# Optimization experiments

Hardware: AMD Instinct MI355X
Metric: run time of the kernel (lower is better)

Reference implementation:

```python
import jax, jax.numpy as jnp
import numpy as np

N = 50000      # nodes
E = 800000     # edges
D = 128        # hidden dim (args.dim) == num_features
B = 5          # GIN blocks
G = 512        # graphs in batch
C = 10         # classes
EPS_GIN = 128.0  # GINConv(nn, in_channels) -> eps = in_channels = 128 (faithful to source)
BN_EPS = 1e-5


def setup_inputs() -> dict:
    key = jax.random.key(0)
    ks = jax.random.split(key, 12)
    xav = 0.1  # ~xavier_uniform std for 128x128
    x = jax.random.normal(ks[0], (N, D), jnp.float32)
    edge_index = jax.random.randint(ks[1], (2, E), 0, N, dtype=jnp.int64)
    batch = jax.random.randint(ks[2], (N,), 0, G, dtype=jnp.int64)
    return dict(
        x=x, edge_index=edge_index, batch=batch,
        W1=jax.random.normal(ks[3], (B, D, D), jnp.float32) * xav,
        b1=jnp.zeros((B, D), jnp.float32),
        g1=jnp.ones((B, D), jnp.float32),
        be1=jnp.zeros((B, D), jnp.float32),
        W2=jax.random.normal(ks[4], (B, D, D), jnp.float32) * xav,
        b2=jnp.zeros((B, D), jnp.float32),
        g2=jnp.ones((B, D), jnp.float32),
        be2=jnp.zeros((B, D), jnp.float32),
        bn_g=jnp.ones((B * D,), jnp.float32),
        bn_b=jnp.zeros((B * D,), jnp.float32),
        Wc1=jax.random.normal(ks[5], (B * D, D), jnp.float32) * 0.05,
        bc1=jnp.zeros((D,), jnp.float32),
        Wc2=jax.random.normal(ks[6], (D, C), jnp.float32) * 0.1,
        bc2=jnp.zeros((C,), jnp.float32),
    )


def _bn(h, g, b):
    # training-mode BatchNorm1d: biased variance over the batch (node/graph) dim
    mu = h.mean(axis=0)
    var = h.var(axis=0)
    return g * (h - mu) * jax.lax.rsqrt(var + BN_EPS) + b


def reference(x, edge_index, batch, W1, b1, g1, be1, W2, b2, g2, be2,
              bn_g, bn_b, Wc1, bc1, Wc2, bc2):
    src, dst = edge_index[0], edge_index[1]
    feats = []
    for i in range(B):
        # GIN aggregation: out[dst] += x[src]
        agg = jax.ops.segment_sum(x[src], dst, num_segments=N)   # [N, D]
        h = (1.0 + EPS_GIN) * x + agg
        h = _bn(jax.nn.relu(h @ W1[i] + b1[i]), g1[i], be1[i])
        h = _bn(jax.nn.relu(h @ W2[i] + b2[i]), g2[i], be2[i])
        x = h
        # global_add_pool per graph
        feats.append(jax.ops.segment_sum(x, batch, num_segments=G))  # [G, D]
    f = jnp.concatenate(feats, axis=1)          # [G, B*D]
    f = _bn(f, bn_g, bn_b)
    f = jax.nn.relu(f @ Wc1 + bc1)              # dropout p=0 (eval)
    logits = f @ Wc2 + bc2                      # [G, C]
    return jax.nn.log_softmax(logits, axis=-1)
```

## Files before the change

kernel.cpp:

```cpp
#include <hip/hip_runtime.h>
#include <hip/hip_bf16.h>

#define NN 50000
#define NE 800000
#define DD 128
#define NB 5
#define NG 512
#define NC 10
#define BN_EPS 1e-5f
#define EPS1 129.0f
#define GATHER_BLOCKS 12500

typedef __hip_bfloat16 bf16;
typedef __attribute__((ext_vector_type(8))) short short8;
typedef __attribute__((ext_vector_type(4))) float f32x4;

__device__ __forceinline__ float b2f(const bf16 v) { return __bfloat162float(v); }
__device__ __forceinline__ float us2f(unsigned int s) {
    return __uint_as_float((s & 0xffffu) << 16);
}
__device__ __forceinline__ unsigned pack2(float a, float b) {
    union { bf16 h; unsigned short u; } ua, ub;
    ua.h = __float2bfloat16(a); ub.h = __float2bfloat16(b);
    return ((unsigned)ub.u << 16) | (unsigned)ua.u;
}
__device__ __forceinline__ short f2bfs(float f) {
    union { bf16 h; short s; } u; u.h = __float2bfloat16(f); return u.s;
}

#define OFF_AGGH   0
#define OFF_XF     3200000
#define OFF_H1     6400000
#define OFF_FEATS  9600000
#define OFF_CSA    9927680
#define OFF_CSB    9927936
#define OFF_SC6    9928192
#define OFF_SH6    9928832
#define OFF_FLAGS  9929472
#define OFF_PARAMS 9929480
#define OFF_DEG    10055680
#define OFF_OFFS   10105680
#define OFF_ELIST  10155712
#define OFF_BDEG   10955712
#define OFF_BOFFS  10956224
#define OFF_RANK   10956800
#define OFF_PART   11006800
#define OFF_ERANK  11006864

#define P_W1T  0
#define P_W2T  81920
#define P_WC1  163840
#define P_B1   245760
#define P_G1   246400
#define P_BE1  247040
#define P_B2   247680
#define P_G2   248320
#define P_BE2  248960
#define P_BNG  249600
#define P_BNB  250240
#define P_BC1  250880
#define P_WC2  251008
#define P_BC2  252288

struct SmallSrc { const void* s[11]; };

__global__ void k_detect(const unsigned* __restrict__ xw, const int* __restrict__ eiw,
                         const int* __restrict__ bw, int* flags, int* __restrict__ bdeg) {
    __shared__ int sh[3];
    const int t = threadIdx.x;
    bdeg[t] = 0; bdeg[256 + t] = 0;
    if (t < 3) sh[t] = 0;
    __syncthreads();
    int c = 0;
    for (int i = 0; i < 16; i++) {
        unsigned w = xw[t * 16 + i];
        unsigned e = (w >> 7) & 0xff;
        c += (e >= 110 && e <= 131) ? 1 : 0;
    }
    atomicAdd(&sh[0], c);
    atomicAdd(&sh[1], (eiw[2 * t + 1] != 0) ? 1 : 0);
    atomicAdd(&sh[2], (bw[2 * t + 1] != 0) ? 1 : 0);
    __syncthreads();
    if (t == 0) {
        flags[0] = (sh[0] > 2048) ? 1 : 0;
        flags[1] = (sh[1] < 8) ? 1 : 0;
        flags[2] = (sh[2] < 8) ? 1 : 0;
    }
}

__global__ void k_bhist(const int* __restrict__ flags, const int* __restrict__ batch,
                        int* __restrict__ bdeg, int* __restrict__ deg) {
    int n = blockIdx.x * 256 + threadIdx.x;
    if (n >= NN) return;
    deg[n] = 0;
    int g = flags[2] ? batch[2 * n] : batch[n];
    atomicAdd(&bdeg[g], 1);
}

__launch_bounds__(512)
__global__ void k_bscan(int* __restrict__ bdeg, int* __restrict__ boffs) {
    __shared__ int part[512];
    const int t = threadIdx.x;
    int d0 = bdeg[t];
    part[t] = d0;
    __syncthreads();
    for (int d = 1; d < 512; d <<= 1) {
        int v = (t >= d) ? part[t - d] : 0;
        __syncthreads();
        part[t] += v;
        __syncthreads();
    }
    int ex = part[t] - d0;
    boffs[t] = ex;
    bdeg[t] = ex;
    if (t == 511) boffs[512] = part[511];
}

__global__ void k_bplace(const int* __restrict__ flags, const int* __restrict__ batch,
                         int* __restrict__ bcur, int* __restrict__ rank) {
    int n = blockIdx.x * 256 + threadIdx.x;
    if (n >= NN) return;
    int g = flags[2] ? batch[2 * n] : batch[n];
    rank[n] = atomicAdd(&bcur[g], 1);
}

__global__ void k_convert_x(const int* __restrict__ flags, const void* __restrict__ xr,
                            const int* __restrict__ rank, bf16* __restrict__ xfh) {
    int i = blockIdx.x * 256 + threadIdx.x;
    int r = i >> 4, seg = i & 15;
    uint4 o;
    if (flags[0]) {
        o = ((const uint4*)xr)[i];
    } else {
        float4 a = ((const float4*)xr)[2 * i], b = ((const float4*)xr)[2 * i + 1];
        o.x = pack2(a.x, a.y); o.y = pack2(a.z, a.w);
        o.z = pack2(b.x, b.y); o.w = pack2(b.z, b.w);
    }
    ((uint4*)xfh)[(long)rank[r] * 16 + seg] = o;
}

__global__ void k_convert_params(const int* __restrict__ flags, const void* w1,
                                 const void* w2, const void* wc1, SmallSrc srcs,
                                 bf16* __restrict__ pb) {
    int i = blockIdx.x * 256 + threadIdx.x;
    if (i < 245760) {
        int which = i / 81920, j = i % 81920;
        const void* src = (which == 0) ? w1 : (which == 1) ? w2 : wc1;
        float v = flags[0] ? us2f(((const unsigned short*)src)[j]) : ((const float*)src)[j];
        if (which == 2) {
            pb[P_WC1 + j] = __float2bfloat16(v);
        } else {
            int layer = j >> 14, rem = j & 16383;
            int k = rem >> 7, c = rem & 127;
            bf16* dst = pb + (which == 0 ? P_W1T : P_W2T);
            dst[(layer << 14) + c * DD + k] = __float2bfloat16(v);
        }
    } else {
        int j = i - 245760;
        if (j >= 6538) return;
        int seg, off;
        if (j < 5120)      { seg = j / 640; off = j - seg * 640; }
        else if (j < 5248) { seg = 8;  off = j - 5120; }
        else if (j < 6528) { seg = 9;  off = j - 5248; }
        else               { seg = 10; off = j - 6528; }
        const void* s = srcs.s[seg];
        float v = flags[0] ? us2f(((const unsigned short*)s)[off]) : ((const float*)s)[off];
        pb[P_B1 + j] = __float2bfloat16(v);
    }
}

__global__ void k_hist(const int* __restrict__ flags, const int* __restrict__ ei,
                       const int* __restrict__ rank, int* __restrict__ deg,
                       int* __restrict__ erank) {
    int e = blockIdx.x * 256 + threadIdx.x;
    int d = flags[1] ? ei[2 * NE + 2 * e] : ei[NE + e];
    erank[e] = atomicAdd(&deg[rank[d]], 1);
}

__global__ void k_scan_part(const int* __restrict__ deg, int* __restrict__ part) {
    __shared__ int red[256];
    const int b = blockIdx.x, t = threadIdx.x;
    int i0 = b * 1024 + t * 4;
    int s = 0;
    if (i0 + 3 < NN) {
        int4 v = *(const int4*)(deg + i0);
        s = v.x + v.y + v.z + v.w;
    } else {
        for (int k = 0; k < 4; k++) if (i0 + k < NN) s += deg[i0 + k];
    }
    red[t] = s;
    __syncthreads();
    for (int d = 128; d > 0; d >>= 1) {
        if (t < d) red[t] += red[t + d];
        __syncthreads();
    }
    if (t == 0) part[b] = red[0];
}

__global__ void k_scan_apply(const int* __restrict__ deg, const int* __restrict__ part,
                             int* __restrict__ offs) {
    __shared__ int red[256];
    __shared__ int base_sh, total_sh;
    const int b = blockIdx.x, t = threadIdx.x;
    if (t < 64) {
        int v = (t < 49) ? part[t] : 0;
        int s = v;
        for (int d = 1; d < 64; d <<= 1) {
            int x = __shfl_up(s, d);
            if (t >= d) s += x;
        }
        if (t == b)  base_sh = s - v;
        if (t == 48) total_sh = s;
    }
    int i0 = b * 1024 + t * 4;
    int v[4]; int s = 0;
    #pragma unroll
    for (int k = 0; k < 4; k++) {
        int idx = i0 + k;
        v[k] = (idx < NN) ? deg[idx] : 0;
        s += v[k];
    }
    red[t] = s;
    __syncthreads();
    for (int d = 1; d < 256; d <<= 1) {
        int x = (t >= d) ? red[t - d] : 0;
        __syncthreads();
        red[t] += x;
        __syncthreads();
    }
    if (b == 0 && t == 0) offs[NN] = total_sh;
    int pre = base_sh + ((t == 0) ? 0 : red[t - 1]);
    #pragma unroll
    for (int k = 0; k < 4; k++) {
        int idx = i0 + k;
        if (idx < NN) { offs[idx] = pre; pre += v[k]; }
    }
}

__global__ void k_place(const int* __restrict__ flags, const int* __restrict__ ei,
                        const int* __restrict__ rank, const int* __restrict__ offs,
                        const int* __restrict__ erank, int* __restrict__ elist) {
    int e = blockIdx.x * 256 + threadIdx.x;
    int s, d;
    if (flags[1]) { s = ei[2 * e]; d = ei[2 * NE + 2 * e]; }
    else          { s = ei[e];     d = ei[NE + e]; }
    elist[offs[rank[d]] + erank[e]] = rank[s];
}

__device__ __forceinline__ void pool_body(int g, int t, const bf16* __restrict__ xfh,
                                          const int* __restrict__ boffs,
                                          const float* __restrict__ csB,
                                          const bf16* __restrict__ g2,
                                          const bf16* __restrict__ be2,
                                          float* __restrict__ feats_blk) {
    __shared__ float2 red[3][64];
    const int l = t & 63;
    const int h = t >> 6;
    const int lo = boffs[g], hi = boffs[g + 1];
    const unsigned* xw = (const unsigned*)xfh;
    float s0 = 0.f, s1 = 0.f;
    for (int n = lo + h; n < hi; n += 4) {
        unsigned p = xw[(long)n * 64 + l];
        s0 += us2f(p); s1 += us2f(p >> 16);
    }
    if (h) red[h - 1][l] = make_float2(s0, s1);
    __syncthreads();
    if (h == 0) {
        s0 += red[0][l].x + red[1][l].x + red[2][l].x;
        s1 += red[0][l].y + red[1][l].y + red[2][l].y;
        int c = l * 2;
        float mu0 = csB[c] * (1.f / NN);
        float var0 = csB[128 + c] * (1.f / NN) - mu0 * mu0;
        float sc0 = b2f(g2[c]) * rsqrtf(var0 + BN_EPS);
        float sh0 = b2f(be2[c]) - mu0 * sc0;
        float mu1 = csB[c + 1] * (1.f / NN);
        float var1 = csB[128 + c + 1] * (1.f / NN) - mu1 * mu1;
        float sc1 = b2f(g2[c + 1]) * rsqrtf(var1 + BN_EPS);
        float sh1 = b2f(be2[c + 1]) - mu1 * sc1;
        float cnt = (float)(hi - lo);
        float* fp = feats_blk + (long)g * (NB * DD) + c;
        fp[0] = sc0 * s0 + cnt * sh0;
        fp[1] = sc1 * s1 + cnt * sh1;
    }
}

__global__ void k_gather_pool(const int* __restrict__ offs, const int* __restrict__ elist,
                              const bf16* __restrict__ xfh, bf16* __restrict__ aggh,
                              const float* __restrict__ csB, const bf16* __restrict__ g2,
                              const bf16* __restrict__ be2, float* __restrict__ csA_zero,
                              const int* __restrict__ boffs, float* __restrict__ feats_prev) {
    if (blockIdx.x >= GATHER_BLOCKS) {
        if (feats_prev)
            pool_body(blockIdx.x - GATHER_BLOCKS, threadIdx.x, xfh, boffs,
                      csB, g2, be2, feats_prev);
        return;
    }
    if (blockIdx.x == 0) csA_zero[threadIdx.x] = 0.f;
    const int w = threadIdx.x >> 6;
    const int lane = threadIdx.x & 63;
    const int half = lane >> 5;
    const int ql = lane & 31;
    const int n = blockIdx.x * 4 + w;
    const int base = offs[n], end = offs[n + 1];
    const uint2* xw2 = (const uint2*)xfh;

    float a0, a1, a2, a3;
    {
        uint2 sp = xw2[(long)n * 32 + ql];
        float m = (half == 0) ? EPS1 : 0.f;
        a0 = m * us2f(sp.x); a1 = m * us2f(sp.x >> 16);
        a2 = m * us2f(sp.y); a3 = m * us2f(sp.y >> 16);
    }

    for (int i = base; i < end; i += 64) {
        int cnt = min(64, end - i);
        int e = (i + lane < end) ? elist[i + lane] : 0;
        int j = 0;
        for (; j + 16 <= cnt; j += 16) {
            uint2 p[8];
            #pragma unroll
            for (int q = 0; q < 8; q++) {
                int sj = __shfl(e, j + 2 * q + half);
                p[q] = xw2[(long)sj * 32 + ql];
            }
            #pragma unroll
            for (int q = 0; q < 8; q++) {
                a0 += us2f(p[q].x); a1 += us2f(p[q].x >> 16);
                a2 += us2f(p[q].y); a3 += us2f(p[q].y >> 16);
            }
        }
        for (; j + 2 <= cnt; j += 2) {
            int sj = __shfl(e, j + half);
            uint2 p = xw2[(long)sj * 32 + ql];
            a0 += us2f(p.x); a1 += us2f(p.x >> 16);
            a2 += us2f(p.y); a3 += us2f(p.y >> 16);
        }
        if (j < cnt && half == 0) {
            int sj = __shfl(e, j);
            uint2 p = xw2[(long)sj * 32 + ql];
            a0 += us2f(p.x); a1 += us2f(p.x >> 16);
            a2 += us2f(p.y); a3 += us2f(p.y >> 16);
        }
    }
    a0 += __shfl_xor(a0, 32); a1 += __shfl_xor(a1, 32);
    a2 += __shfl_xor(a2, 32); a3 += __shfl_xor(a3, 32);

    if (csB) {
        int c = ql * 4;
        float fac = (float)(end - base) + EPS1;
        #pragma unroll
        for (int k = 0; k < 4; k++) {
            float mu = csB[c + k] * (1.f / NN);
            float var = csB[128 + c + k] * (1.f / NN) - mu * mu;
            float sc = b2f(g2[c + k]) * rsqrtf(var + BN_EPS);
            float sh = b2f(be2[c + k]) - mu * sc;
            float* ap = (k == 0) ? &a0 : (k == 1) ? &a1 : (k == 2) ? &a2 : &a3;
            *ap = sc * (*ap) + fac * sh;
        }
    }
    if (half == 0)
        ((uint2*)aggh)[(long)n * 32 + ql] = make_uint2(pack2(a0, a1), pack2(a2, a3));
}

__launch_bounds__(256)
__global__ void k_pool(const bf16* __restrict__ xfh, const int* __restrict__ boffs,
                       const float* __restrict__ csB, const bf16* __restrict__ g2,
                       const bf16* __restrict__ be2, float* __restrict__ feats_blk) {
    pool_body(blockIdx.x, threadIdx.x, xfh, boffs, csB, g2, be2, feats_blk);
}

#define WS_S 136
__launch_bounds__(512)
__global__ void k_gemm_mfma(const bf16* __restrict__ A, const bf16* __restrict__ WT,
                            const bf16* __restrict__ bias,
                            const float* __restrict__ bn_cs, const bf16* __restrict__ bn_g,
                            const bf16* __restrict__ bn_be,
                            bf16* __restrict__ Out, float* __restrict__ cs_out,
                            float* cs_zero) {
    __shared__ short Ws[128 * WS_S];
    __shared__ float s_cs[256];
    __shared__ float s_sc[DD], s_sh[DD];
    const int t = threadIdx.x;
    const int row0 = blockIdx.x * 128;

    if (t < 256) {
        if (cs_zero && blockIdx.x == 0) cs_zero[t] = 0.f;
        s_cs[t] = 0.f;
    }
    if (bn_cs && t < DD) {
        float mu = bn_cs[t] * (1.f / NN);
        float var = bn_cs[128 + t] * (1.f / NN) - mu * mu;
        float sc = b2f(bn_g[t]) * rsqrtf(var + BN_EPS);
        s_sc[t] = sc;
        s_sh[t] = b2f(bn_be[t]) - mu * sc;
    }
    {
        const uint4* Wg = (const uint4*)WT;
        #pragma unroll
        for (int i = 0; i < 4; i++) {
            int idx = i * 512 + t;
            int row = idx >> 4, seg = idx & 15;
            *(uint4*)(&Ws[row * WS_S + seg * 8]) = Wg[idx];
        }
    }
    __syncthreads();

    const int w = t >> 6;
    const int lane = t & 63;
    const int m = lane & 15;
    const int half = lane >> 4;
    const int r = row0 + w * 16 + m;

    short8 afrag[4];
    if (r < NN) {
        #pragma unroll
        for (int kk = 0; kk < 4; kk++)
            afrag[kk] = *(const short8*)(A + (long)r * DD + kk * 32 + half * 8);
        if (bn_cs) {
            #pragma unroll
            for (int kk = 0; kk < 4; kk++) {
                int c0 = kk * 32 + half * 8;
                uint4 p = *(uint4*)&afrag[kk];
                float v0 = us2f(p.x) * s_sc[c0+0] + s_sh[c0+0];
                float v1 = us2f(p.x >> 16) * s_sc[c0+1] + s_sh[c0+1];
                float v2 = us2f(p.y) * s_sc[c0+2] + s_sh[c0+2];
                float v3 = us2f(p.y >> 16) * s_sc[c0+3] + s_sh[c0+3];
                float v4 = us2f(p.z) * s_sc[c0+4] + s_sh[c0+4];
                float v5 = us2f(p.z >> 16) * s_sc[c0+5] + s_sh[c0+5];
                float v6 = us2f(p.w) * s_sc[c0+6] + s_sh[c0+6];
                float v7 = us2f(p.w >> 16) * s_sc[c0+7] + s_sh[c0+7];
                p.x = pack2(v0, v1); p.y = pack2(v2, v3);
                p.z = pack2(v4, v5); p.w = pack2(v6, v7);
                afrag[kk] = *(short8*)&p;
            }
        }
    } else {
        #pragma unroll
        for (int kk = 0; kk < 4; kk++) afrag[kk] = (short8){0,0,0,0,0,0,0,0};
    }

    f32x4 acc[8];
    #pragma unroll
    for (int nt = 0; nt < 8; nt++) acc[nt] = (f32x4){0.f, 0.f, 0.f, 0.f};

    #pragma unroll
    for (int nt = 0; nt < 8; nt++) {
        const short* wrow = &Ws[(nt * 16 + m) * WS_S + half * 8];
        #pragma unroll
        for (int kk = 0; kk < 4; kk++) {
            short8 b = *(const short8*)(wrow + kk * 32);
            acc[nt] = __builtin_amdgcn_mfma_f32_16x16x32_bf16(afrag[kk], b, acc[nt], 0, 0, 0);
        }
    }

    __syncthreads();
    short* Cs = Ws;
    #pragma unroll
    for (int nt = 0; nt < 8; nt++) {
        int col = nt * 16 + m;
        float bi = b2f(bias[col]);
        float ps = 0.f, pq = 0.f;
        #pragma unroll
        for (int reg = 0; reg < 4; reg++) {
            int rr = row0 + w * 16 + half * 4 + reg;
            float o = fmaxf(acc[nt][reg] + bi, 0.f);
            Cs[(w * 16 + half * 4 + reg) * WS_S + col] = f2bfs(o);
            if (rr < NN) { ps += o; pq += o * o; }
        }
        ps += __shfl_xor(ps, 16); ps += __shfl_xor(ps, 32);
        pq += __shfl_xor(pq, 16); pq += __shfl_xor(pq, 32);
        if (half == 0) {
            atomicAdd(&s_cs[col], ps);
            atomicAdd(&s_cs[128 + col], pq);
        }
    }
    __syncthreads();
    #pragma unroll
    for (int i = 0; i < 4; i++) {
        int idx = i * 512 + t;
        int row = idx >> 4, seg = idx & 15;
        int rr = row0 + row;
        if (rr < NN)
            *(uint4*)(Out + (long)rr * DD + seg * 8) = *(uint4*)(&Cs[row * WS_S + seg * 8]);
    }
    if (t < 256) atomicAdd(&cs_out[t], s_cs[t]);
}

__global__ void k_feat_stats(const float* __restrict__ feats, const bf16* __restrict__ bn_g,
                             const bf16* __restrict__ bn_b, float* __restrict__ sc6,
                             float* __restrict__ sh6) {
    int j = blockIdx.x * 256 + threadIdx.x;
    if (j >= NB * DD) return;
    float s = 0.f, sq = 0.f;
    for (int g = 0; g < NG; g++) {
        float v = feats[(long)g * (NB * DD) + j];
        s += v; sq += v * v;
    }
    float mu = s / NG;
    float var = sq / NG - mu * mu;
    float sc = b2f(bn_g[j]) * rsqrtf(var + BN_EPS);
    sc6[j] = sc;
    sh6[j] = b2f(bn_b[j]) - mu * sc;
}

__launch_bounds__(128)
__global__ void k_head(const int* __restrict__ flags, const float* __restrict__ feats,
                       const float* __restrict__ sc6, const float* __restrict__ sh6,
                       const bf16* __restrict__ Wc1, const bf16* __restrict__ bc1,
                       const bf16* __restrict__ Wc2, const bf16* __restrict__ bc2,
                       void* out) {
    __shared__ float fs[NB * DD];
    __shared__ float f1[DD];
    __shared__ float lg[NC + 2];
    const int g = blockIdx.x, t = threadIdx.x;
    for (int j = t; j < NB * DD; j += 128)
        fs[j] = feats[(long)g * (NB * DD) + j] * sc6[j] + sh6[j];
    __syncthreads();
    float acc = b2f(bc1[t]);
    for (int j = 0; j < NB * DD; j++) acc += fs[j] * b2f(Wc1[j * DD + t]);
    f1[t] = fmaxf(acc, 0.f);
    __syncthreads();
    if (t < NC) {
        float a = b2f(bc2[t]);
        for (int k = 0; k < DD; k++) a += f1[k] * b2f(Wc2[k * NC + t]);
        lg[t] = a;
    }
    __syncthreads();
    if (t == 0) {
        float m = -1e30f;
        for (int c = 0; c < NC; c++) m = fmaxf(m, lg[c]);
        float s = 0.f;
        for (int c = 0; c < NC; c++) s += expf(lg[c] - m);
        lg[NC] = m + logf(s);
    }
    __syncthreads();
    if (t < NC) {
        float val = lg[t] - lg[NC];
        if (flags[0]) ((bf16*)out)[g * NC + t] = __float2bfloat16(val);
        else          ((float*)out)[g * NC + t] = val;
    }
}

extern "C" void kernel_launch(void* const* d_in, const int* in_sizes, int n_in,
                              void* d_out, int out_size, void* d_ws, size_t ws_size,
                              hipStream_t stream) {
    const void* x     = d_in[0];
    const int*  ei    = (const int*)d_in[1];
    const int*  batch = (const int*)d_in[2];

    float* ws    = (float*)d_ws;
    bf16*  aggh  = (bf16*)(ws + OFF_AGGH);
    bf16*  xfh   = (bf16*)(ws + OFF_XF);
    bf16*  h1h   = (bf16*)(ws + OFF_H1);
    float* feats = ws + OFF_FEATS;
    float* csA   = ws + OFF_CSA;
    float* csB   = ws + OFF_CSB;
    float* sc6   = ws + OFF_SC6;
    float* sh6   = ws + OFF_SH6;
    int*   flags = (int*)(ws + OFF_FLAGS);
    bf16*  pb    = (bf16*)(ws + OFF_PARAMS);
    int*   deg   = (int*)(ws + OFF_DEG);
    int*   offs  = (int*)(ws + OFF_OFFS);
    int*   elist = (int*)(ws + OFF_ELIST);
    int*   bdeg  = (int*)(ws + OFF_BDEG);
    int*   boffs = (int*)(ws + OFF_BOFFS);
    int*   rank  = (int*)(ws + OFF_RANK);
    int*   part  = (int*)(ws + OFF_PART);
    int*   erank = (int*)(ws + OFF_ERANK);

    bf16 *pW1T = pb + P_W1T, *pW2T = pb + P_W2T, *pWc1 = pb + P_WC1;
    bf16 *pb1 = pb + P_B1, *pg1 = pb + P_G1, *pbe1 = pb + P_BE1;
    bf16 *pb2 = pb + P_B2, *pg2 = pb + P_G2, *pbe2 = pb + P_BE2;
    bf16 *pbng = pb + P_BNG, *pbnb = pb + P_BNB;
    bf16 *pbc1 = pb + P_BC1, *pWc2 = pb + P_WC2, *pbc2 = pb + P_BC2;

    k_detect<<<1, 256, 0, stream>>>((const unsigned*)x, ei, batch, flags, bdeg);

    k_bhist<<<(NN + 255) / 256, 256, 0, stream>>>(flags, batch, bdeg, deg);
    k_bscan<<<1, 512, 0, stream>>>(bdeg, boffs);
    k_bplace<<<(NN + 255) / 256, 256, 0, stream>>>(flags, batch, bdeg, rank);

    k_convert_x<<<NN * DD / 8 / 256, 256, 0, stream>>>(flags, x, rank, xfh);

    SmallSrc ss;
    ss.s[0] = d_in[4];  ss.s[1] = d_in[5];  ss.s[2] = d_in[6];
    ss.s[3] = d_in[8];  ss.s[4] = d_in[9];  ss.s[5] = d_in[10];
    ss.s[6] = d_in[11]; ss.s[7] = d_in[12];
    ss.s[8] = d_in[14]; ss.s[9] = d_in[15]; ss.s[10] = d_in[16];
    k_convert_params<<<(245760 + 6538 + 255) / 256, 256, 0, stream>>>(
        flags, d_in[3], d_in[7], d_in[13], ss, pb);

    k_hist<<<NE / 256, 256, 0, stream>>>(flags, ei, rank, deg, erank);
    k_scan_part<<<49, 256, 0, stream>>>(deg, part);
    k_scan_apply<<<49, 256, 0, stream>>>(deg, part, offs);
    k_place<<<NE / 256, 256, 0, stream>>>(flags, ei, rank, offs, erank, elist);

    const int gemm_blocks = (NN + 127) / 128;
    for (int i = 0; i < NB; i++) {
        k_gather_pool<<<GATHER_BLOCKS + NG, 256, 0, stream>>>(
            offs, elist, xfh, aggh,
            (i == 0) ? nullptr : csB,
            pg2 + (i - 1) * DD, pbe2 + (i - 1) * DD, csA,
            boffs, (i == 0) ? nullptr : feats + (i - 1) * DD);
        k_gemm_mfma<<<gemm_blocks, 512, 0, stream>>>(aggh, pW1T + i * DD * DD, pb1 + i * DD,
                                                     nullptr, nullptr, nullptr,
                                                     h1h, csA, csB);
        k_gemm_mfma<<<gemm_blocks, 512, 0, stream>>>(h1h, pW2T + i * DD * DD, pb2 + i * DD,
                                                     csA, pg1 + i * DD, pbe1 + i * DD,
                                                     xfh, csB, nullptr);
    }
    k_pool<<<NG, 256, 0, stream>>>(xfh, boffs, csB, pg2 + (NB - 1) * DD,
                                   pbe2 + (NB - 1) * DD, feats + (NB - 1) * DD);

    k_feat_stats<<<3, 256, 0, stream>>>(feats, pbng, pbnb, sc6, sh6);
    k_head<<<NG, 128, 0, stream>>>(flags, feats, sc6, sh6, pWc1, pbc1, pWc2, pbc2, d_out);
}
```

Measured before the change: 656.4 us.

## Fuse the two per-block GEMMs with a grid barrier for BatchNorm statistics

Merges the two MLP GEMM kernels of each GIN block into one kernel. The intermediate activation stays in shared memory, and a global atomic-counter barrier waits for the first BatchNorm's column statistics to be complete before the second GEMM runs. This removes one kernel launch and the h1 global-memory round trip per block, but the spin barrier relies on all 391 blocks being resident at once, which is what the launch-bounds occupancy hint targets. It also parallelizes the feature-statistics reduction across more blocks and transposes Wc1 so the head reads it with vectorized loads.

```diff
diff --git a/kernel.cpp b/kernel.cpp
--- a/kernel.cpp
+++ b/kernel.cpp
@@ -85,6 +85,7 @@
         flags[0] = (sh[0] > 2048) ? 1 : 0;
         flags[1] = (sh[1] < 8) ? 1 : 0;
         flags[2] = (sh[2] < 8) ? 1 : 0;
+        flags[6] = 0;
     }
 }
 
@@ -148,7 +149,8 @@
         const void* src = (which == 0) ? w1 : (which == 1) ? w2 : wc1;
         float v = flags[0] ? us2f(((const unsigned short*)src)[j]) : ((const float*)src)[j];
         if (which == 2) {
-            pb[P_WC1 + j] = __float2bfloat16(v);
+            int rowj = j >> 7, col = j & 127;
+            pb[P_WC1 + col * (NB * DD) + rowj] = __float2bfloat16(v);
         } else {
             int layer = j >> 14, rem = j & 16383;
             int k = rem >> 7, c = rem & 127;
@@ -370,37 +372,32 @@
 }
 
 #define WS_S 136
-__launch_bounds__(512)
-__global__ void k_gemm_mfma(const bf16* __restrict__ A, const bf16* __restrict__ WT,
-                            const bf16* __restrict__ bias,
-                            const float* __restrict__ bn_cs, const bf16* __restrict__ bn_g,
-                            const bf16* __restrict__ bn_be,
-                            bf16* __restrict__ Out, float* __restrict__ cs_out,
-                            float* cs_zero) {
-    __shared__ short Ws[128 * WS_S];
+__launch_bounds__(512, 4)
+__global__ void k_gemm_fused(const bf16* __restrict__ A,
+                             const bf16* __restrict__ W1T, const bf16* __restrict__ W2T,
+                             const bf16* __restrict__ b1v, const bf16* __restrict__ g1v,
+                             const bf16* __restrict__ be1v, const bf16* __restrict__ b2v,
+                             bf16* __restrict__ Out,
+                             float* __restrict__ csA,
+                             float* __restrict__ csB,
+                             int* __restrict__ ctr, int target) {
+    __shared__ short Ws1[128 * WS_S];
+    __shared__ short Ws2[128 * WS_S];
     __shared__ float s_cs[256];
     __shared__ float s_sc[DD], s_sh[DD];
     const int t = threadIdx.x;
     const int row0 = blockIdx.x * 128;
 
-    if (t < 256) {
-        if (cs_zero && blockIdx.x == 0) cs_zero[t] = 0.f;
-        s_cs[t] = 0.f;
-    }
-    if (bn_cs && t < DD) {
-        float mu = bn_cs[t] * (1.f / NN);
-        float var = bn_cs[128 + t] * (1.f / NN) - mu * mu;
-        float sc = b2f(bn_g[t]) * rsqrtf(var + BN_EPS);
-        s_sc[t] = sc;
-        s_sh[t] = b2f(bn_be[t]) - mu * sc;
-    }
+    if (t < 256) s_cs[t] = 0.f;
     {
-        const uint4* Wg = (const uint4*)WT;
+        const uint4* Wg1 = (const uint4*)W1T;
+        const uint4* Wg2 = (const uint4*)W2T;
         #pragma unroll
         for (int i = 0; i < 4; i++) {
             int idx = i * 512 + t;
             int row = idx >> 4, seg = idx & 15;
-            *(uint4*)(&Ws[row * WS_S + seg * 8]) = Wg[idx];
+            *(uint4*)(&Ws1[row * WS_S + seg * 8]) = Wg1[idx];
+            *(uint4*)(&Ws2[row * WS_S + seg * 8]) = Wg2[idx];
         }
     }
     __syncthreads();
@@ -416,24 +413,6 @@
         #pragma unroll
         for (int kk = 0; kk < 4; kk++)
             afrag[kk] = *(const short8*)(A + (long)r * DD + kk * 32 + half * 8);
-        if (bn_cs) {
-            #pragma unroll
-            for (int kk = 0; kk < 4; kk++) {
-                int c0 = kk * 32 + half * 8;
-                uint4 p = *(uint4*)&afrag[kk];
-                float v0 = us2f(p.x) * s_sc[c0+0] + s_sh[c0+0];
-                float v1 = us2f(p.x >> 16) * s_sc[c0+1] + s_sh[c0+1];
-                float v2 = us2f(p.y) * s_sc[c0+2] + s_sh[c0+2];
-                float v3 = us2f(p.y >> 16) * s_sc[c0+3] + s_sh[c0+3];
-                float v4 = us2f(p.z) * s_sc[c0+4] + s_sh[c0+4];
-                float v5 = us2f(p.z >> 16) * s_sc[c0+5] + s_sh[c0+5];
-                float v6 = us2f(p.w) * s_sc[c0+6] + s_sh[c0+6];
-                float v7 = us2f(p.w >> 16) * s_sc[c0+7] + s_sh[c0+7];
-                p.x = pack2(v0, v1); p.y = pack2(v2, v3);
-                p.z = pack2(v4, v5); p.w = pack2(v6, v7);
-                afrag[kk] = *(short8*)&p;
-            }
-        }
     } else {
         #pragma unroll
         for (int kk = 0; kk < 4; kk++) afrag[kk] = (short8){0,0,0,0,0,0,0,0};
@@ -442,10 +421,9 @@
     f32x4 acc[8];
     #pragma unroll
     for (int nt = 0; nt < 8; nt++) acc[nt] = (f32x4){0.f, 0.f, 0.f, 0.f};
-
     #pragma unroll
     for (int nt = 0; nt < 8; nt++) {
-        const short* wrow = &Ws[(nt * 16 + m) * WS_S + half * 8];
+        const short* wrow = &Ws1[(nt * 16 + m) * WS_S + half * 8];
         #pragma unroll
         for (int kk = 0; kk < 4; kk++) {
             short8 b = *(const short8*)(wrow + kk * 32);
@@ -454,11 +432,87 @@
     }
 
     __syncthreads();
-    short* Cs = Ws;
+    short* Cs = Ws1;
     #pragma unroll
     for (int nt = 0; nt < 8; nt++) {
         int col = nt * 16 + m;
-        float bi = b2f(bias[col]);
+        float bi = b2f(b1v[col]);
+        float ps = 0.f, pq = 0.f;
+        #pragma unroll
+        for (int reg = 0; reg < 4; reg++) {
+            int rr = row0 + w * 16 + half * 4 + reg;
+            float o = fmaxf(acc[nt][reg] + bi, 0.f);
+            Cs[(w * 16 + half * 4 + reg) * WS_S + col] = f2bfs(o);
+            if (rr < NN) { ps += o; pq += o * o; }
+        }
+        ps += __shfl_xor(ps, 16); ps += __shfl_xor(ps, 32);
+        pq += __shfl_xor(pq, 16); pq += __shfl_xor(pq, 32);
+        if (half == 0) {
+            atomicAdd(&s_cs[col], ps);
+            atomicAdd(&s_cs[128 + col], pq);
+        }
+    }
+    __syncthreads();
+    if (t < 256) atomicAdd(&csA[t], s_cs[t]);
+    if (blockIdx.x == 0 && t < 256)
+        atomicExch(&csB[t], 0.f);
+    __syncthreads();
+
+    if (t == 0) {
+        __threadfence();
+        atomicAdd(ctr, 1);
+        while (__hip_atomic_load(ctr, __ATOMIC_ACQUIRE, __HIP_MEMORY_SCOPE_AGENT) < target) {
+            __builtin_amdgcn_s_sleep(2);
+        }
+    }
+    __syncthreads();
+
+    if (t < DD) {
+        float su = __hip_atomic_load(&csA[t], __ATOMIC_RELAXED, __HIP_MEMORY_SCOPE_AGENT);
+        float sq = __hip_atomic_load(&csA[128 + t], __ATOMIC_RELAXED, __HIP_MEMORY_SCOPE_AGENT);
+        float mu = su * (1.f / NN);
+        float var = sq * (1.f / NN) - mu * mu;
+        float sc = b2f(g1v[t]) * rsqrtf(var + BN_EPS);
+        s_sc[t] = sc;
+        s_sh[t] = b2f(be1v[t]) - mu * sc;
+        s_cs[t] = 0.f; s_cs[128 + t] = 0.f;
+    }
+    __syncthreads();
+
+    #pragma unroll
+    for (int kk = 0; kk < 4; kk++) {
+        int c0 = kk * 32 + half * 8;
+        short8 raw = *(const short8*)(&Cs[(w * 16 + m) * WS_S + c0]);
+        uint4 p = *(uint4*)&raw;
+        float v0 = us2f(p.x) * s_sc[c0+0] + s_sh[c0+0];
+        float v1 = us2f(p.x >> 16) * s_sc[c0+1] + s_sh[c0+1];
+        float v2 = us2f(p.y) * s_sc[c0+2] + s_sh[c0+2];
+        float v3 = us2f(p.y >> 16) * s_sc[c0+3] + s_sh[c0+3];
+        float v4 = us2f(p.z) * s_sc[c0+4] + s_sh[c0+4];
+        float v5 = us2f(p.z >> 16) * s_sc[c0+5] + s_sh[c0+5];
+        float v6 = us2f(p.w) * s_sc[c0+6] + s_sh[c0+6];
+        float v7 = us2f(p.w >> 16) * s_sc[c0+7] + s_sh[c0+7];
+        p.x = pack2(v0, v1); p.y = pack2(v2, v3);
+        p.z = pack2(v4, v5); p.w = pack2(v6, v7);
+        afrag[kk] = *(short8*)&p;
+    }
+
+    #pragma unroll
+    for (int nt = 0; nt < 8; nt++) acc[nt] = (f32x4){0.f, 0.f, 0.f, 0.f};
+    #pragma unroll
+    for (int nt = 0; nt < 8; nt++) {
+        const short* wrow = &Ws2[(nt * 16 + m) * WS_S + half * 8];
+        #pragma unroll
+        for (int kk = 0; kk < 4; kk++) {
+            short8 b = *(const short8*)(wrow + kk * 32);
+            acc[nt] = __builtin_amdgcn_mfma_f32_16x16x32_bf16(afrag[kk], b, acc[nt], 0, 0, 0);
+        }
+    }
+
+    #pragma unroll
+    for (int nt = 0; nt < 8; nt++) {
+        int col = nt * 16 + m;
+        float bi = b2f(b2v[col]);
         float ps = 0.f, pq = 0.f;
         #pragma unroll
         for (int reg = 0; reg < 4; reg++) {
@@ -483,30 +537,39 @@
         if (rr < NN)
             *(uint4*)(Out + (long)rr * DD + seg * 8) = *(uint4*)(&Cs[row * WS_S + seg * 8]);
     }
-    if (t < 256) atomicAdd(&cs_out[t], s_cs[t]);
-}
-
+    if (t < 256) atomicAdd(&csB[t], s_cs[t]);
+}
+
+__launch_bounds__(256)
 __global__ void k_feat_stats(const float* __restrict__ feats, const bf16* __restrict__ bn_g,
                              const bf16* __restrict__ bn_b, float* __restrict__ sc6,
                              float* __restrict__ sh6) {
-    int j = blockIdx.x * 256 + threadIdx.x;
-    if (j >= NB * DD) return;
-    float s = 0.f, sq = 0.f;
-    for (int g = 0; g < NG; g++) {
-        float v = feats[(long)g * (NB * DD) + j];
-        s += v; sq += v * v;
-    }
-    float mu = s / NG;
-    float var = sq / NG - mu * mu;
-    float sc = b2f(bn_g[j]) * rsqrtf(var + BN_EPS);
-    sc6[j] = sc;
-    sh6[j] = b2f(bn_b[j]) - mu * sc;
+    __shared__ float rs[8][32], rq[8][32];
+    const int j0 = blockIdx.x * 32;
+    const int jl = threadIdx.x & 31, gg = threadIdx.x >> 5;
+    float s = 0.f, q = 0.f;
+    for (int g = gg; g < NG; g += 8) {
+        float v = feats[(long)g * (NB * DD) + j0 + jl];
+        s += v; q += v * v;
+    }
+    rs[gg][jl] = s; rq[gg][jl] = q;
+    __syncthreads();
+    if (gg == 0) {
+        #pragma unroll
+        for (int k = 1; k < 8; k++) { s += rs[k][jl]; q += rq[k][jl]; }
+        int j = j0 + jl;
+        float mu = s / NG;
+        float var = q / NG - mu * mu;
+        float sc = b2f(bn_g[j]) * rsqrtf(var + BN_EPS);
+        sc6[j] = sc;
+        sh6[j] = b2f(bn_b[j]) - mu * sc;
+    }
 }
 
 __launch_bounds__(128)
 __global__ void k_head(const int* __restrict__ flags, const float* __restrict__ feats,
                        const float* __restrict__ sc6, const float* __restrict__ sh6,
-                       const bf16* __restrict__ Wc1, const bf16* __restrict__ bc1,
+                       const bf16* __restrict__ Wc1T, const bf16* __restrict__ bc1,
                        const bf16* __restrict__ Wc2, const bf16* __restrict__ bc2,
                        void* out) {
     __shared__ float fs[NB * DD];
@@ -517,7 +580,20 @@
         fs[j] = feats[(long)g * (NB * DD) + j] * sc6[j] + sh6[j];
     __syncthreads();
     float acc = b2f(bc1[t]);
-    for (int j = 0; j < NB * DD; j++) acc += fs[j] * b2f(Wc1[j * DD + t]);
+    {
+        const short8* wr = (const short8*)(Wc1T + (long)t * (NB * DD));
+        #pragma unroll 4
+        for (int jb = 0; jb < 80; jb++) {
+            short8 wv = wr[jb];
+            uint4 p = *(uint4*)&wv;
+            float4 f0 = *(const float4*)&fs[jb * 8];
+            float4 f1v = *(const float4*)&fs[jb * 8 + 4];
+            acc += f0.x * us2f(p.x) + f0.y * us2f(p.x >> 16)
+                 + f0.z * us2f(p.y) + f0.w * us2f(p.y >> 16)
+                 + f1v.x * us2f(p.z) + f1v.y * us2f(p.z >> 16)
+                 + f1v.z * us2f(p.w) + f1v.w * us2f(p.w >> 16);
+        }
+    }
     f1[t] = fmaxf(acc, 0.f);
     __syncthreads();
     if (t < NC) {
@@ -551,7 +627,6 @@
     float* ws    = (float*)d_ws;
     bf16*  aggh  = (bf16*)(ws + OFF_AGGH);
     bf16*  xfh   = (bf16*)(ws + OFF_XF);
-    bf16*  h1h   = (bf16*)(ws + OFF_H1);
     float* feats = ws + OFF_FEATS;
     float* csA   = ws + OFF_CSA;
     float* csB   = ws + OFF_CSB;
@@ -573,6 +648,7 @@
     bf16 *pb2 = pb + P_B2, *pg2 = pb + P_G2, *pbe2 = pb + P_BE2;
     bf16 *pbng = pb + P_BNG, *pbnb = pb + P_BNB;
     bf16 *pbc1 = pb + P_BC1, *pWc2 = pb + P_WC2, *pbc2 = pb + P_BC2;
+    int*  ctr  = flags + 6;
 
     k_detect<<<1, 256, 0, stream>>>((const unsigned*)x, ei, batch, flags, bdeg);
 
@@ -602,16 +678,14 @@
             (i == 0) ? nullptr : csB,
             pg2 + (i - 1) * DD, pbe2 + (i - 1) * DD, csA,
             boffs, (i == 0) ? nullptr : feats + (i - 1) * DD);
-        k_gemm_mfma<<<gemm_blocks, 512, 0, stream>>>(aggh, pW1T + i * DD * DD, pb1 + i * DD,
-                                                     nullptr, nullptr, nullptr,
-                                                     h1h, csA, csB);
-        k_gemm_mfma<<<gemm_blocks, 512, 0, stream>>>(h1h, pW2T + i * DD * DD, pb2 + i * DD,
-                                                     csA, pg1 + i * DD, pbe1 + i * DD,
-                                                     xfh, csB, nullptr);
+        k_gemm_fused<<<gemm_blocks, 512, 0, stream>>>(
+            aggh, pW1T + i * DD * DD, pW2T + i * DD * DD,
+            pb1 + i * DD, pg1 + i * DD, pbe1 + i * DD, pb2 + i * DD,
+            xfh, csA, csB, ctr, (i + 1) * gemm_blocks);
     }
     k_pool<<<NG, 256, 0, stream>>>(xfh, boffs, csB, pg2 + (NB - 1) * DD,
                                    pbe2 + (NB - 1) * DD, feats + (NB - 1) * DD);
 
-    k_feat_stats<<<3, 256, 0, stream>>>(feats, pbng, pbnb, sc6, sh6);
+    k_feat_stats<<<20, 256, 0, stream>>>(feats, pbng, pbnb, sc6, sh6);
     k_head<<<NG, 128, 0, stream>>>(flags, feats, sc6, sh6, pWc1, pbc1, pWc2, pbc2, d_out);
 }
```

Result: slower. 789.7 us (+20.3%).
